# Optimization experiments

Measured on AMD Instinct MI355X. Metric: run time of the kernel, lower is better.

## Reference

```python
import jax, jax.numpy as jnp
import numpy as np

HEADS, DK, DV, STRIDE = 8, 32, 32, 2
EPS = 1e-5

def dwconv(x, w, b, stride):
    # depthwise 3x3, padding 1; w: [C,1,3,3]
    y = jax.lax.conv_general_dilated(
        x, w, (stride, stride), ((1, 1), (1, 1)),
        dimension_numbers=("NCHW", "OIHW", "NCHW"),
        feature_group_count=x.shape[1])
    return y + b[None, :, None, None]

def setup_inputs() -> dict:
    key = jax.random.key(0)
    ks = jax.random.split(key, 16)
    B_, C, H, W = 8, 256, 56, 56
    hd = HEADS * DK
    s = lambda k, shp: (jax.random.normal(k, shp, jnp.float32) * 0.02)
    return {
        "x": jax.random.normal(ks[0], (B_, C, H, W), jnp.float32),
        "Wk_dw": s(ks[1], (C, 1, 3, 3)), "bk_dw": jnp.zeros((C,), jnp.float32),
        "Wv_dw": s(ks[2], (C, 1, 3, 3)), "bv_dw": jnp.zeros((C,), jnp.float32),
        "Wq": s(ks[3], (hd, C)), "bq": jnp.zeros((hd,), jnp.float32),
        "Wk": s(ks[4], (hd, C)), "bk": jnp.zeros((hd,), jnp.float32),
        "Wv": s(ks[5], (HEADS * DV, C)), "bv": jnp.zeros((HEADS * DV,), jnp.float32),
        "Wo": s(ks[6], (C, HEADS * DV)), "bo": jnp.zeros((C,), jnp.float32),
        "Bbias": s(ks[7], (1, HEADS, H * W, (H // STRIDE) * (W // STRIDE))),
    }

def reference(x, Wk_dw, bk_dw, Wv_dw, bv_dw, Wq, bq, Wk, bk, Wv, bv, Wo, bo, Bbias):
    b, c, h, w = x.shape
    xr = x.reshape(b, c, h * w).transpose(0, 2, 1)  # [b, hw, c]
    # F.layer_norm with normalized_shape=(b, hw, c): single mean/var over ALL elements
    mu = jnp.mean(xr)
    var = jnp.mean((xr - mu) ** 2)
    xn = (xr - mu) * jax.lax.rsqrt(var + EPS)
    q = (xn @ Wq.T + bq).reshape(b, h * w, HEADS, DK).transpose(0, 2, 1, 3)  # [b,H,hw,dk]
    ki = dwconv(x, Wk_dw, bk_dw, STRIDE)
    kh, kw = ki.shape[2], ki.shape[3]
    kf = ki.reshape(b, c, kh * kw).transpose(0, 2, 1)
    k = (kf @ Wk.T + bk).reshape(b, kh * kw, HEADS, DK).transpose(0, 2, 1, 3)
    vi = dwconv(x, Wv_dw, bv_dw, STRIDE)
    vf = vi.reshape(b, c, kh * kw).transpose(0, 2, 1)
    v = (vf @ Wv.T + bv).reshape(b, kh * kw, HEADS, DV).transpose(0, 2, 1, 3)
    attn = jnp.einsum("bhid,bhjd->bhij", q, k) * (DK ** -0.5) + Bbias
    attn = jax.nn.softmax(attn, axis=-1)
    res = jnp.einsum("bhij,bhjd->bhid", attn, v).transpose(0, 2, 1, 3)
    res = res.reshape(b, h * w, HEADS * DV)
    out = (res @ Wo.T + bo).reshape(b, c, h, w)  # faithful to original .view (no transpose)
    return out + x
```

## Files before the change

### kernel.cpp

```cpp
#include <hip/hip_runtime.h>

typedef unsigned short u16;
typedef unsigned int   u32;
typedef __attribute__((ext_vector_type(8))) short short8;
typedef __attribute__((ext_vector_type(4))) float f32x4;

#define MFMA16(a, b, c) __builtin_amdgcn_mfma_f32_16x16x32_bf16((a), (b), (c), 0, 0, 0)

static constexpr int B_ = 8;
static constexpr int HW = 3136;
static constexpr int KW = 784;
static constexpr int NELEM = B_ * 256 * HW;

static constexpr size_t OFF_CNT = 4096;
static constexpr size_t OFF_W   = 8192;
static constexpr int AOFF_WQ = 0, AOFF_WK = 65536, AOFF_WV = 131072, AOFF_WO = 196608;
static constexpr int AOFF_WKDW = 262144, AOFF_WVDW = 264448;
static constexpr int AOFF_BKDW = 266752, AOFF_BVDW = 267008, AOFF_BQ = 267264;
static constexpr int AOFF_BK = 267520, AOFF_BV = 267776, AOFF_BO = 268032;
static constexpr size_t OFF_XT  = 557056;
static constexpr size_t SZ_XT   = (size_t)B_ * HW * 256 * 2;
static constexpr size_t SZ_KJ   = (size_t)B_ * KW * 256 * 2;
static constexpr size_t OFF_KIT = OFF_XT + SZ_XT;
static constexpr size_t OFF_VIT = OFF_KIT + SZ_KJ;
static constexpr size_t OFF_KI  = OFF_VIT + SZ_KJ;
static constexpr size_t OFF_VI  = OFF_KI + SZ_KJ;
static constexpr size_t OFF_Q   = OFF_VI + SZ_KJ;
static constexpr size_t OFF_O   = OFF_XT;

__device__ __forceinline__ float bf2f(u16 u) { return __uint_as_float(((u32)u) << 16); }
__device__ __forceinline__ u16 f2bf(float f) {
  u32 u = __float_as_uint(f);
  u32 r = u + 0x7FFFu + ((u >> 16) & 1u);
  return (u16)(r >> 16);
}
__device__ __forceinline__ float bflo(u32 u) { return __uint_as_float(u << 16); }
__device__ __forceinline__ float bfhi(u32 u) { return __uint_as_float(u & 0xFFFF0000u); }
__device__ __forceinline__ u32 packbf(float a, float b) {
  u32 ua = __float_as_uint(a); ua = (ua + 0x7FFFu + ((ua >> 16) & 1u)) >> 16;
  u32 ub = __float_as_uint(b); ub = (ub + 0x7FFFu + ((ub >> 16) & 1u)) >> 16;
  return ua | (ub << 16);
}

__global__ __launch_bounds__(256) void detect_k(const u32* __restrict__ x, int* __restrict__ cnt) {
  int c = 0;
  for (int i = threadIdx.x; i < 4096; i += 256) {
    float v = __uint_as_float(x[i] << 16);
    if (fabsf(v) > 1e4f) c++;
  }
#pragma unroll
  for (int off = 32; off > 0; off >>= 1) c += __shfl_down(c, off);
  if ((threadIdx.x & 63) == 0) atomicAdd(cnt, c);
}

struct CvtArgs { const void* src[12]; int dstoff[12]; int n[12]; };
__global__ __launch_bounds__(256) void cvtw_k(CvtArgs a, u16* __restrict__ arena,
                                              const int* __restrict__ cnt) {
  int t = blockIdx.y;
  int n = a.n[t];
  u16* d = arena + a.dstoff[t];
  int f32m = (*cnt >= 64);
  if (f32m) {
    const float* s = (const float*)a.src[t];
    for (int i = blockIdx.x * 256 + threadIdx.x; i < n; i += gridDim.x * 256) d[i] = f2bf(s[i]);
  } else {
    const u16* s = (const u16*)a.src[t];
    for (int i = blockIdx.x * 256 + threadIdx.x; i < n; i += gridDim.x * 256) d[i] = s[i];
  }
}

__global__ __launch_bounds__(256) void reduce_k(const void* __restrict__ x, double* __restrict__ acc,
                                                const int* __restrict__ cnt) {
  int f32m = (*cnt >= 64);
  float s = 0.f, ss = 0.f;
  if (f32m) {
    const float4* xv = (const float4*)x;
    const int n4 = NELEM / 4;
    for (int i = blockIdx.x * 256 + threadIdx.x; i < n4; i += gridDim.x * 256) {
      float4 u = xv[i];
      s += u.x + u.y + u.z + u.w;
      ss += u.x * u.x + u.y * u.y + u.z * u.z + u.w * u.w;
    }
  } else {
    const uint4* xv = (const uint4*)x;
    const int n8 = NELEM / 8;
    for (int i = blockIdx.x * 256 + threadIdx.x; i < n8; i += gridDim.x * 256) {
      uint4 u = xv[i];
      u32 w[4] = {u.x, u.y, u.z, u.w};
#pragma unroll
      for (int q = 0; q < 4; q++) {
        float f0 = __uint_as_float(w[q] << 16);
        float f1 = __uint_as_float(w[q] & 0xFFFF0000u);
        s += f0 + f1;
        ss += f0 * f0 + f1 * f1;
      }
    }
  }
#pragma unroll
  for (int off = 32; off > 0; off >>= 1) {
    s += __shfl_down(s, off);
    ss += __shfl_down(ss, off);
  }
  __shared__ float as_[4], ass_[4];
  int wv = threadIdx.x >> 6;
  if ((threadIdx.x & 63) == 0) { as_[wv] = s; ass_[wv] = ss; }
  __syncthreads();
  if (threadIdx.x == 0) {
    atomicAdd(acc + 0, (double)(as_[0] + as_[1] + as_[2] + as_[3]));
    atomicAdd(acc + 1, (double)(ass_[0] + ass_[1] + ass_[2] + ass_[3]));
  }
}

__global__ __launch_bounds__(256) void prep_k(const u16* __restrict__ wq, const u16* __restrict__ bq,
                                              float* __restrict__ wsf) {
  const double* acc = (const double*)wsf;
  __shared__ float sh[2];
  if (threadIdx.x == 0) {
    double N = (double)NELEM;
    double mu = acc[0] / N;
    double var = acc[1] / N - mu * mu;
    float rstd = (float)(1.0 / sqrt(var + 1e-5));
    sh[0] = (float)mu; sh[1] = rstd;
    wsf[4] = (float)mu; wsf[5] = rstd;
    wsf[6] = rstd * 0.17677669529663687f;
  }
  __syncthreads();
  int o = threadIdx.x;
  float wsum = 0.f;
  for (int c = 0; c < 256; c++) wsum += bf2f(wq[o * 256 + c]);
  wsf[16 + o] = (bf2f(bq[o]) - sh[1] * sh[0] * wsum) * 0.17677669529663687f;
}

__global__ __launch_bounds__(256) void transpose_x_k(const void* __restrict__ src, u16* __restrict__ dst,
                                                     const int* __restrict__ cnt) {
  int f32m = (*cnt >= 64);
  __shared__ u16 t[32][33];
  int b = blockIdx.z;
  int r0 = blockIdx.y * 32, c0 = blockIdx.x * 32;
  int tid = threadIdx.x, col = tid & 31;
  size_t base = (size_t)b * 256 * HW;
  if (f32m) {
    const float* s = (const float*)src + base;
#pragma unroll
    for (int i = 0; i < 4; i++) {
      int row = (tid >> 5) + i * 8;
      t[row][col] = f2bf(s[(size_t)(r0 + row) * HW + c0 + col]);
    }
  } else {
    const u16* s = (const u16*)src + base;
#pragma unroll
    for (int i = 0; i < 4; i++) {
      int row = (tid >> 5) + i * 8;
      t[row][col] = s[(size_t)(r0 + row) * HW + c0 + col];
    }
  }
  __syncthreads();
  u16* d = dst + base;
#pragma unroll
  for (int i = 0; i < 4; i++) {
    int row = (tid >> 5) + i * 8;
    d[(size_t)(c0 + row) * 256 + r0 + col] = t[col][row];
  }
}

__global__ __launch_bounds__(256) void transpose_kv_k(const u16* __restrict__ s1, u16* __restrict__ d1,
                                                      const u16* __restrict__ s2, u16* __restrict__ d2) {
  __shared__ u16 t[32][33];
  int which = blockIdx.z >> 3;
  int b = blockIdx.z & 7;
  const u16* src = which ? s2 : s1;
  u16* dst = which ? d2 : d1;
  int r0 = blockIdx.y * 32, c0 = blockIdx.x * 32;
  const u16* s = src + (size_t)b * 256 * KW;
  u16* d = dst + (size_t)b * 256 * KW;
  int tid = threadIdx.x, col = tid & 31;
#pragma unroll
  for (int i = 0; i < 4; i++) {
    int row = (tid >> 5) + i * 8;
    if (c0 + col < KW) t[row][col] = s[(size_t)(r0 + row) * KW + c0 + col];
  }
  __syncthreads();
#pragma unroll
  for (int i = 0; i < 4; i++) {
    int row = (tid >> 5) + i * 8;
    if (c0 + row < KW) d[(size_t)(c0 + row) * 256 + r0 + col] = t[col][row];
  }
}

__global__ __launch_bounds__(256) void dwconv_k(const void* __restrict__ x,
                                                const u16* __restrict__ arena,
                                                u16* __restrict__ ki, u16* __restrict__ vi,
                                                const int* __restrict__ cnt) {
  int f32m = (*cnt >= 64);
  int b = blockIdx.x >> 8;
  int c = blockIdx.x & 255;
  float wkf[9], wvf[9];
#pragma unroll
  for (int t = 0; t < 9; t++) {
    wkf[t] = bf2f(arena[AOFF_WKDW + c * 9 + t]);
    wvf[t] = bf2f(arena[AOFF_WVDW + c * 9 + t]);
  }
  float kb = bf2f(arena[AOFF_BKDW + c]), vb = bf2f(arena[AOFF_BVDW + c]);
  size_t xbase = (size_t)(b * 256 + c) * HW;
  auto body = [&](auto LDX) {
    for (int j = threadIdx.x; j < KW; j += 256) {
      int oi = j / 28, oj = j % 28;
      float ka = kb, va = vb;
#pragma unroll
      for (int di = 0; di < 3; di++) {
        int ii = 2 * oi - 1 + di;
        if ((unsigned)ii >= 56u) continue;
#pragma unroll
        for (int dj = 0; dj < 3; dj++) {
          int ij = 2 * oj - 1 + dj;
          if ((unsigned)ij >= 56u) continue;
          float xv = LDX(ii * 56 + ij);
          ka += xv * wkf[di * 3 + dj];
          va += xv * wvf[di * 3 + dj];
        }
      }
      ki[(size_t)(b * 256 + c) * KW + j] = f2bf(ka);
      vi[(size_t)(b * 256 + c) * KW + j] = f2bf(va);
    }
  };
  if (f32m) {
    const float* xp = (const float*)x + xbase;
    body([&](int i) { return xp[i]; });
  } else {
    const u16* xp = (const u16*)x + xbase;
    body([&](int i) { return bf2f(xp[i]); });
  }
}

template<int MODE>
__global__ __launch_bounds__(256, 4) void proj2_k(const u16* __restrict__ act, const u16* __restrict__ Wt,
                                                  const float* __restrict__ wsf, const u16* __restrict__ bias,
                                                  const void* __restrict__ x, void* __restrict__ outp,
                                                  const int* __restrict__ cnt, int R, int tpb) {
  __shared__ __align__(16) u16 Wl[64 * 264];
  int tid = threadIdx.x, lane = tid & 63, wave = tid >> 6;
  int l15 = lane & 15, quad = lane >> 4;
  int og = blockIdx.x & 3;
  int tmp = blockIdx.x >> 2;
  int qc = tmp % 7, b = tmp / 7;
  {
    int row = tid >> 2, cb = (tid & 3) * 64;
    const u16* wsrc = Wt + (size_t)(og * 64 + row) * 256 + cb;
#pragma unroll
    for (int i = 0; i < 8; i++)
      *(short8*)&Wl[row * 264 + cb + i * 8] = *(const short8*)(wsrc + i * 8);
  }
  __syncthreads();
  int f32m = (MODE == 2) ? (*cnt >= 64) : 0;
  float alpha = (MODE == 0) ? wsf[6] : 0.f;
  for (int tt = wave; tt < tpb; tt += 4) {
    int p0 = (qc * tpb + tt) * 16;
    const u16* arow = act + ((size_t)b * R + p0 + l15) * 256 + quad * 8;
    short8 afr[8];
#pragma unroll
    for (int ks = 0; ks < 8; ks++) afr[ks] = *(const short8*)(arow + ks * 32);
#pragma unroll
    for (int ot = 0; ot < 4; ot++) {
      f32x4 acc = {0.f, 0.f, 0.f, 0.f};
#pragma unroll
      for (int ks = 0; ks < 8; ks++) {
        short8 bfr = *(const short8*)&Wl[(ot * 16 + l15) * 264 + ks * 32 + quad * 8];
        acc = MFMA16(afr[ks], bfr, acc);
      }
      int o = og * 64 + ot * 16 + l15;
      if (MODE == 0) {
        float bet = wsf[16 + o];
        u16* q = (u16*)outp;
#pragma unroll
        for (int r = 0; r < 4; r++)
          q[((size_t)b * R + p0 + quad * 4 + r) * 256 + o] = f2bf(alpha * acc[r] + bet);
      } else if (MODE == 1) {
        float bi = bf2f(bias[o]);
        u16* ko = (u16*)outp;
#pragma unroll
        for (int r = 0; r < 4; r++)
          ko[((size_t)b * R + p0 + quad * 4 + r) * 256 + o] = f2bf(acc[r] + bi);
      } else {
        float bi = bf2f(bias[o]);
        if (f32m) {
          const float* xf = (const float*)x;
          float* of = (float*)outp;
#pragma unroll
          for (int r = 0; r < 4; r++) {
            size_t idx = ((size_t)b * R + p0 + quad * 4 + r) * 256 + o;
            of[idx] = acc[r] + bi + xf[idx];
          }
        } else {
          const u16* xb = (const u16*)x;
          u16* ob_ = (u16*)outp;
#pragma unroll
          for (int r = 0; r < 4; r++) {
            size_t idx = ((size_t)b * R + p0 + quad * 4 + r) * 256 + o;
            ob_[idx] = f2bf(acc[r] + bi + bf2f(xb[idx]));
          }
        }
      }
    }
  }
}

__global__ __launch_bounds__(256) void proj_v_k(const u16* __restrict__ Wv, const u16* __restrict__ vit,
                                                const u16* __restrict__ bv, u16* __restrict__ vT) {
  int lane = threadIdx.x & 63, wave = threadIdx.x >> 6;
  int l15 = lane & 15, quad = lane >> 4;
  int b = blockIdx.x >> 4;
  int ob = (blockIdx.x >> 2) & 3;
  int js = blockIdx.x & 3;
  int o0 = ob * 64 + wave * 16;
  const u16* arow = Wv + (size_t)(o0 + l15) * 256 + quad * 8;
  short8 af[8];
#pragma unroll
  for (int ks = 0; ks < 8; ks++) af[ks] = *(const short8*)(arow + ks * 32);
  int jt0 = js * 13;
  int jt1 = (jt0 + 13 < 49) ? jt0 + 13 : 49;
  for (int jt = jt0; jt < jt1; jt++) {
    const u16* brow = vit + ((size_t)(b * KW) + jt * 16 + l15) * 256 + quad * 8;
    f32x4 acc = {0.f, 0.f, 0.f, 0.f};
#pragma unroll
    for (int ks = 0; ks < 8; ks++) acc = MFMA16(af[ks], *(const short8*)(brow + ks * 32), acc);
#pragma unroll
    for (int r = 0; r < 4; r++) {
      int o = o0 + quad * 4 + r;
      vT[((size_t)(b * 256) + o) * KW + jt * 16 + l15] = f2bf(acc[r] + bf2f(bv[o]));
    }
  }
}

static constexpr int PSTRIDE = 136;
__global__ __launch_bounds__(256, 3) void attn_k(const u16* __restrict__ q, const u16* __restrict__ k,
                                                 const u16* __restrict__ vT, const void* __restrict__ Bb,
                                                 u16* __restrict__ Ob, const int* __restrict__ cnt) {
  int f32m = (*cnt >= 64);
  int tid = threadIdx.x;
  int lane = tid & 63, wave = tid >> 6;
  int l15 = lane & 15, quad = lane >> 4;
  int bid = blockIdx.x;
  int pt = bid >> 4;
  int h = (bid >> 1) & 7;
  int half = bid & 1;
  int b = half * 4 + wave;
  int p0 = pt * 16;
  __shared__ __align__(16) u16 blsT[784 * 16];
  __shared__ __align__(16) u16 Pch[4][16 * PSTRIDE];

  {
    size_t boff = ((size_t)(h * HW) + p0) * KW;
    if (f32m) {
      const float* bbf = (const float*)Bb + boff;
#pragma unroll
      for (int it = 0; it < 13; it++) {
        int chunk = it * 256 + tid;
        if (chunk < 3136) {
          int row = chunk / 196, c4 = (chunk - row * 196) * 4;
          float4 v = *(const float4*)(bbf + (size_t)row * KW + c4);
          blsT[(c4 + 0) * 16 + row] = f2bf(v.x);
          blsT[(c4 + 1) * 16 + row] = f2bf(v.y);
          blsT[(c4 + 2) * 16 + row] = f2bf(v.z);
          blsT[(c4 + 3) * 16 + row] = f2bf(v.w);
        }
      }
    } else {
      const u16* bbb = (const u16*)Bb + boff;
#pragma unroll
      for (int it = 0; it < 13; it++) {
        int chunk = it * 256 + tid;
        if (chunk < 3136) {
          int row = chunk / 196, c4 = (chunk - row * 196) * 4;
          uint2 lv = *(const uint2*)(bbb + (size_t)row * KW + c4);
          blsT[(c4 + 0) * 16 + row] = (u16)(lv.x & 0xFFFFu);
          blsT[(c4 + 1) * 16 + row] = (u16)(lv.x >> 16);
          blsT[(c4 + 2) * 16 + row] = (u16)(lv.y & 0xFFFFu);
          blsT[(c4 + 3) * 16 + row] = (u16)(lv.y >> 16);
        }
      }
    }
  }
  __syncthreads();

  const u16* qp = q + ((size_t)(b * HW) + p0 + l15) * 256 + h * 32 + quad * 8;
  short8 af = *(const short8*)qp;
  const u16* kb = k + (size_t)b * KW * 256 + h * 32 + quad * 8;
  const u16* vb = vT + ((size_t)(b * 256) + h * 32) * KW;
  u16* pw = &Pch[wave][0];

  float m[4], l[4];
  f32x4 oa = {0.f, 0.f, 0.f, 0.f}, oc = {0.f, 0.f, 0.f, 0.f};
#pragma unroll
  for (int r = 0; r < 4; r++) { m[r] = -3.0e38f; l[r] = 0.f; }

#pragma unroll 1
  for (int c = 0; c < 7; c++) {
    f32x4 s[8];
#pragma unroll
    for (int t = 0; t < 8; t++) {
      int jt = c * 8 + t;
      int jrow = jt * 16 + l15;
      int jcl = jrow > 783 ? 783 : jrow;
      short8 kf = *(const short8*)(kb + (size_t)jcl * 256);
      f32x4 acc = {0.f, 0.f, 0.f, 0.f};
      acc = MFMA16(af, kf, acc);
      uint2 braw = *(const uint2*)&blsT[jcl * 16 + quad * 4];
      bool valid = jrow < 784;
      s[t][0] = valid ? acc[0] + bflo(braw.x) : -3.0e38f;
      s[t][1] = valid ? acc[1] + bfhi(braw.x) : -3.0e38f;
      s[t][2] = valid ? acc[2] + bflo(braw.y) : -3.0e38f;
      s[t][3] = valid ? acc[3] + bfhi(braw.y) : -3.0e38f;
    }
    float cm[4], al[4], ps[4];
#pragma unroll
    for (int r = 0; r < 4; r++) {
      float v = s[0][r];
#pragma unroll
      for (int t = 1; t < 8; t++) v = fmaxf(v, s[t][r]);
      cm[r] = v;
    }
#pragma unroll
    for (int off = 1; off < 16; off <<= 1)
#pragma unroll
      for (int r = 0; r < 4; r++) cm[r] = fmaxf(cm[r], __shfl_xor(cm[r], off));
#pragma unroll
    for (int r = 0; r < 4; r++) {
      float mn = fmaxf(m[r], cm[r]);
      al[r] = __expf(m[r] - mn);
      m[r] = mn;
      ps[r] = 0.f;
    }
#pragma unroll
    for (int t = 0; t < 8; t++)
#pragma unroll
      for (int r = 0; r < 4; r++) {
        float e = __expf(s[t][r] - m[r]);
        s[t][r] = e;
        ps[r] += e;
      }
#pragma unroll
    for (int off = 1; off < 16; off <<= 1)
#pragma unroll
      for (int r = 0; r < 4; r++) ps[r] += __shfl_xor(ps[r], off);
#pragma unroll
    for (int r = 0; r < 4; r++) {
      l[r] = l[r] * al[r] + ps[r];
      oa[r] *= al[r];
      oc[r] *= al[r];
    }
#pragma unroll
    for (int t = 0; t < 8; t++) {
      int col = t * 16 + l15;
#pragma unroll
      for (int r = 0; r < 4; r++)
        pw[(quad * 4 + r) * PSTRIDE + col] = f2bf(s[t][r]);
    }
    __builtin_amdgcn_s_waitcnt(0xC07F);
#pragma unroll
    for (int kc = 0; kc < 4; kc++) {
      short8 pf = *(const short8*)(pw + l15 * PSTRIDE + kc * 32 + quad * 8);
      int jo = c * 128 + kc * 32 + quad * 8;
      if (jo > 776) jo = 776;
      short8 v0 = *(const short8*)(vb + (size_t)l15 * KW + jo);
      short8 v1 = *(const short8*)(vb + (size_t)(16 + l15) * KW + jo);
      oa = MFMA16(pf, v0, oa);
      oc = MFMA16(pf, v1, oc);
    }
  }

  size_t obase = ((size_t)(b * HW) + p0 + quad * 4) * 256 + h * 32 + l15;
#pragma unroll
  for (int r = 0; r < 4; r++) {
    float inv = 1.f / l[r];
    Ob[obase + (size_t)r * 256]      = f2bf(oa[r] * inv);
    Ob[obase + (size_t)r * 256 + 16] = f2bf(oc[r] * inv);
  }
}

extern "C" void kernel_launch(void* const* d_in, const int* in_sizes, int n_in,
                              void* d_out, int out_size, void* d_ws, size_t ws_size,
                              hipStream_t stream) {
  (void)in_sizes; (void)n_in; (void)out_size; (void)ws_size;
  const void* x = d_in[0];
  char* ws = (char*)d_ws;
  int* cnt = (int*)(ws + OFF_CNT);
  u16* arena = (u16*)(ws + OFF_W);
  u16* xt  = (u16*)(ws + OFF_XT);
  u16* kit = (u16*)(ws + OFF_KIT);
  u16* vit = (u16*)(ws + OFF_VIT);
  u16* ki  = (u16*)(ws + OFF_KI);
  u16* vi  = (u16*)(ws + OFF_VI);
  u16* qb  = (u16*)(ws + OFF_Q);
  u16* Obuf = (u16*)(ws + OFF_O);

  CvtArgs a;
  const int srcidx[12] = {5, 7, 9, 11, 1, 3, 2, 4, 6, 8, 10, 12};
  const int dofs[12] = {AOFF_WQ, AOFF_WK, AOFF_WV, AOFF_WO, AOFF_WKDW, AOFF_WVDW,
                        AOFF_BKDW, AOFF_BVDW, AOFF_BQ, AOFF_BK, AOFF_BV, AOFF_BO};
  const int ns[12] = {65536, 65536, 65536, 65536, 2304, 2304, 256, 256, 256, 256, 256, 256};
  for (int i = 0; i < 12; i++) { a.src[i] = d_in[srcidx[i]]; a.dstoff[i] = dofs[i]; a.n[i] = ns[i]; }

  hipMemsetAsync(d_ws, 0, 8192, stream);
  detect_k<<<1, 256, 0, stream>>>((const u32*)x, cnt);
  cvtw_k<<<dim3(32, 12), 256, 0, stream>>>(a, arena, cnt);
  reduce_k<<<1024, 256, 0, stream>>>(x, (double*)d_ws, cnt);
  prep_k<<<1, 256, 0, stream>>>(arena + AOFF_WQ, arena + AOFF_BQ, (float*)d_ws);
  transpose_x_k<<<dim3(98, 8, 8), 256, 0, stream>>>(x, xt, cnt);
  dwconv_k<<<2048, 256, 0, stream>>>(x, arena, ki, vi, cnt);
  transpose_kv_k<<<dim3(25, 8, 16), 256, 0, stream>>>(ki, kit, vi, vit);
  proj2_k<1><<<224, 256, 0, stream>>>(kit, arena + AOFF_WK, nullptr, arena + AOFF_BK,
                                      nullptr, ki, cnt, KW, 7);
  proj_v_k<<<128, 256, 0, stream>>>(arena + AOFF_WV, vit, arena + AOFF_BV, vi);
  proj2_k<0><<<224, 256, 0, stream>>>(xt, arena + AOFF_WQ, (const float*)d_ws, nullptr,
                                      nullptr, qb, cnt, HW, 28);
  attn_k<<<3136, 256, 0, stream>>>(qb, ki, vi, d_in[13], Obuf, cnt);
  proj2_k<2><<<224, 256, 0, stream>>>(Obuf, arena + AOFF_WO, nullptr, arena + AOFF_BO,
                                      x, d_out, cnt, HW, 28);
}
```

Before: 531.7 us.

## Fuse stats into transpose, inline dtype detect, drop bias LDS staging in attention

Removes the memset, detect and reduce kernels: the dtype check becomes a per-wave ballot inside each kernel, and the layer-norm sum and sum of squares are computed as block partials in the x transpose and reduced in prep. The attention kernel no longer stages the bias tile transposed in shared memory and instead loads bias directly from global per score. It also raises the attention occupancy hint to 6, writes the softmax probabilities to LDS in the same loop as the exponentials, and doubles the grid for the Q and output projections. Direct strided global bias loads may cost more bandwidth than the staged copy did, in exchange for lower LDS use and higher occupancy.

Result: slower. 780.1 us (+46.7%).

```diff
diff --git a/kernel.cpp b/kernel.cpp
--- a/kernel.cpp
+++ b/kernel.cpp
@@ -2,6 +2,7 @@
 
 typedef unsigned short u16;
 typedef unsigned int   u32;
+typedef unsigned long long u64;
 typedef __attribute__((ext_vector_type(8))) short short8;
 typedef __attribute__((ext_vector_type(4))) float f32x4;
 
@@ -10,15 +11,14 @@
 static constexpr int B_ = 8;
 static constexpr int HW = 3136;
 static constexpr int KW = 784;
-static constexpr int NELEM = B_ * 256 * HW;
-
-static constexpr size_t OFF_CNT = 4096;
-static constexpr size_t OFF_W   = 8192;
+
+static constexpr size_t OFF_PART = 4096;
+static constexpr size_t OFF_W   = 131072;
 static constexpr int AOFF_WQ = 0, AOFF_WK = 65536, AOFF_WV = 131072, AOFF_WO = 196608;
 static constexpr int AOFF_WKDW = 262144, AOFF_WVDW = 264448;
 static constexpr int AOFF_BKDW = 266752, AOFF_BVDW = 267008, AOFF_BQ = 267264;
 static constexpr int AOFF_BK = 267520, AOFF_BV = 267776, AOFF_BO = 268032;
-static constexpr size_t OFF_XT  = 557056;
+static constexpr size_t OFF_XT  = 688128;
 static constexpr size_t SZ_XT   = (size_t)B_ * HW * 256 * 2;
 static constexpr size_t SZ_KJ   = (size_t)B_ * KW * 256 * 2;
 static constexpr size_t OFF_KIT = OFF_XT + SZ_XT;
@@ -36,30 +36,21 @@
 }
 __device__ __forceinline__ float bflo(u32 u) { return __uint_as_float(u << 16); }
 __device__ __forceinline__ float bfhi(u32 u) { return __uint_as_float(u & 0xFFFF0000u); }
-__device__ __forceinline__ u32 packbf(float a, float b) {
-  u32 ua = __float_as_uint(a); ua = (ua + 0x7FFFu + ((ua >> 16) & 1u)) >> 16;
-  u32 ub = __float_as_uint(b); ub = (ub + 0x7FFFu + ((ub >> 16) & 1u)) >> 16;
-  return ua | (ub << 16);
-}
-
-__global__ __launch_bounds__(256) void detect_k(const u32* __restrict__ x, int* __restrict__ cnt) {
-  int c = 0;
-  for (int i = threadIdx.x; i < 4096; i += 256) {
-    float v = __uint_as_float(x[i] << 16);
-    if (fabsf(v) > 1e4f) c++;
-  }
-#pragma unroll
-  for (int off = 32; off > 0; off >>= 1) c += __shfl_down(c, off);
-  if ((threadIdx.x & 63) == 0) atomicAdd(cnt, c);
+
+__device__ __forceinline__ int detect_f32(const u32* __restrict__ ref) {
+  int lane = threadIdx.x & 63;
+  float v = __uint_as_float(ref[lane] << 16);
+  u64 b = __ballot(fabsf(v) > 1e4f);
+  return __popcll(b) >= 4;
 }
 
 struct CvtArgs { const void* src[12]; int dstoff[12]; int n[12]; };
 __global__ __launch_bounds__(256) void cvtw_k(CvtArgs a, u16* __restrict__ arena,
-                                              const int* __restrict__ cnt) {
+                                              const u32* __restrict__ xw) {
+  int f32m = detect_f32(xw);
   int t = blockIdx.y;
   int n = a.n[t];
   u16* d = arena + a.dstoff[t];
-  int f32m = (*cnt >= 64);
   if (f32m) {
     const float* s = (const float*)a.src[t];
     for (int i = blockIdx.x * 256 + threadIdx.x; i < n; i += gridDim.x * 256) d[i] = f2bf(s[i]);
@@ -69,89 +60,33 @@
   }
 }
 
-__global__ __launch_bounds__(256) void reduce_k(const void* __restrict__ x, double* __restrict__ acc,
-                                                const int* __restrict__ cnt) {
-  int f32m = (*cnt >= 64);
-  float s = 0.f, ss = 0.f;
-  if (f32m) {
-    const float4* xv = (const float4*)x;
-    const int n4 = NELEM / 4;
-    for (int i = blockIdx.x * 256 + threadIdx.x; i < n4; i += gridDim.x * 256) {
-      float4 u = xv[i];
-      s += u.x + u.y + u.z + u.w;
-      ss += u.x * u.x + u.y * u.y + u.z * u.z + u.w * u.w;
-    }
-  } else {
-    const uint4* xv = (const uint4*)x;
-    const int n8 = NELEM / 8;
-    for (int i = blockIdx.x * 256 + threadIdx.x; i < n8; i += gridDim.x * 256) {
-      uint4 u = xv[i];
-      u32 w[4] = {u.x, u.y, u.z, u.w};
-#pragma unroll
-      for (int q = 0; q < 4; q++) {
-        float f0 = __uint_as_float(w[q] << 16);
-        float f1 = __uint_as_float(w[q] & 0xFFFF0000u);
-        s += f0 + f1;
-        ss += f0 * f0 + f1 * f1;
-      }
-    }
-  }
-#pragma unroll
-  for (int off = 32; off > 0; off >>= 1) {
-    s += __shfl_down(s, off);
-    ss += __shfl_down(ss, off);
-  }
-  __shared__ float as_[4], ass_[4];
-  int wv = threadIdx.x >> 6;
-  if ((threadIdx.x & 63) == 0) { as_[wv] = s; ass_[wv] = ss; }
-  __syncthreads();
-  if (threadIdx.x == 0) {
-    atomicAdd(acc + 0, (double)(as_[0] + as_[1] + as_[2] + as_[3]));
-    atomicAdd(acc + 1, (double)(ass_[0] + ass_[1] + ass_[2] + ass_[3]));
-  }
-}
-
-__global__ __launch_bounds__(256) void prep_k(const u16* __restrict__ wq, const u16* __restrict__ bq,
-                                              float* __restrict__ wsf) {
-  const double* acc = (const double*)wsf;
-  __shared__ float sh[2];
-  if (threadIdx.x == 0) {
-    double N = (double)NELEM;
-    double mu = acc[0] / N;
-    double var = acc[1] / N - mu * mu;
-    float rstd = (float)(1.0 / sqrt(var + 1e-5));
-    sh[0] = (float)mu; sh[1] = rstd;
-    wsf[4] = (float)mu; wsf[5] = rstd;
-    wsf[6] = rstd * 0.17677669529663687f;
-  }
-  __syncthreads();
-  int o = threadIdx.x;
-  float wsum = 0.f;
-  for (int c = 0; c < 256; c++) wsum += bf2f(wq[o * 256 + c]);
-  wsf[16 + o] = (bf2f(bq[o]) - sh[1] * sh[0] * wsum) * 0.17677669529663687f;
-}
-
 __global__ __launch_bounds__(256) void transpose_x_k(const void* __restrict__ src, u16* __restrict__ dst,
-                                                     const int* __restrict__ cnt) {
-  int f32m = (*cnt >= 64);
+                                                     float2* __restrict__ part) {
+  int f32m = detect_f32((const u32*)src);
   __shared__ u16 t[32][33];
   int b = blockIdx.z;
   int r0 = blockIdx.y * 32, c0 = blockIdx.x * 32;
   int tid = threadIdx.x, col = tid & 31;
   size_t base = (size_t)b * 256 * HW;
+  float s = 0.f, ss = 0.f;
   if (f32m) {
-    const float* s = (const float*)src + base;
+    const float* sp = (const float*)src + base;
 #pragma unroll
     for (int i = 0; i < 4; i++) {
       int row = (tid >> 5) + i * 8;
-      t[row][col] = f2bf(s[(size_t)(r0 + row) * HW + c0 + col]);
+      float v = sp[(size_t)(r0 + row) * HW + c0 + col];
+      t[row][col] = f2bf(v);
+      s += v; ss += v * v;
     }
   } else {
-    const u16* s = (const u16*)src + base;
+    const u16* sp = (const u16*)src + base;
 #pragma unroll
     for (int i = 0; i < 4; i++) {
       int row = (tid >> 5) + i * 8;
-      t[row][col] = s[(size_t)(r0 + row) * HW + c0 + col];
+      u16 raw = sp[(size_t)(r0 + row) * HW + c0 + col];
+      t[row][col] = raw;
+      float v = bf2f(raw);
+      s += v; ss += v * v;
     }
   }
   __syncthreads();
@@ -161,6 +96,52 @@
     int row = (tid >> 5) + i * 8;
     d[(size_t)(c0 + row) * 256 + r0 + col] = t[col][row];
   }
+#pragma unroll
+  for (int off = 32; off > 0; off >>= 1) {
+    s += __shfl_down(s, off);
+    ss += __shfl_down(ss, off);
+  }
+  __shared__ float rs[4], rss[4];
+  if ((tid & 63) == 0) { rs[tid >> 6] = s; rss[tid >> 6] = ss; }
+  __syncthreads();
+  if (tid == 0) {
+    int idx = (blockIdx.z * gridDim.y + blockIdx.y) * gridDim.x + blockIdx.x;
+    part[idx] = make_float2(rs[0] + rs[1] + rs[2] + rs[3], rss[0] + rss[1] + rss[2] + rss[3]);
+  }
+}
+
+__global__ __launch_bounds__(256) void prep_k(const u16* __restrict__ wq, const u16* __restrict__ bq,
+                                              const float2* __restrict__ part, float* __restrict__ wsf) {
+  double s = 0.0, ss = 0.0;
+  for (int i = threadIdx.x; i < 6272; i += 256) {
+    float2 p = part[i];
+    s += (double)p.x; ss += (double)p.y;
+  }
+#pragma unroll
+  for (int off = 32; off > 0; off >>= 1) {
+    s += __shfl_down(s, off);
+    ss += __shfl_down(ss, off);
+  }
+  __shared__ double ds[4], dss[4];
+  __shared__ float sh[2];
+  int tid = threadIdx.x;
+  if ((tid & 63) == 0) { ds[tid >> 6] = s; dss[tid >> 6] = ss; }
+  __syncthreads();
+  if (tid == 0) {
+    double S = ds[0] + ds[1] + ds[2] + ds[3];
+    double SS = dss[0] + dss[1] + dss[2] + dss[3];
+    double N = (double)B_ * 256 * HW;
+    double mu = S / N;
+    double var = SS / N - mu * mu;
+    float rstd = (float)(1.0 / sqrt(var + 1e-5));
+    sh[0] = (float)mu; sh[1] = rstd;
+    wsf[6] = rstd * 0.17677669529663687f;
+  }
+  __syncthreads();
+  int o = tid;
+  float wsum = 0.f;
+  for (int c = 0; c < 256; c++) wsum += bf2f(wq[o * 256 + c]);
+  wsf[16 + o] = (bf2f(bq[o]) - sh[1] * sh[0] * wsum) * 0.17677669529663687f;
 }
 
 __global__ __launch_bounds__(256) void transpose_kv_k(const u16* __restrict__ s1, u16* __restrict__ d1,
@@ -189,9 +170,8 @@
 
 __global__ __launch_bounds__(256) void dwconv_k(const void* __restrict__ x,
                                                 const u16* __restrict__ arena,
-                                                u16* __restrict__ ki, u16* __restrict__ vi,
-                                                const int* __restrict__ cnt) {
-  int f32m = (*cnt >= 64);
+                                                u16* __restrict__ ki, u16* __restrict__ vi) {
+  int f32m = detect_f32((const u32*)x);
   int b = blockIdx.x >> 8;
   int c = blockIdx.x & 255;
   float wkf[9], wvf[9];
@@ -236,13 +216,13 @@
 __global__ __launch_bounds__(256, 4) void proj2_k(const u16* __restrict__ act, const u16* __restrict__ Wt,
                                                   const float* __restrict__ wsf, const u16* __restrict__ bias,
                                                   const void* __restrict__ x, void* __restrict__ outp,
-                                                  const int* __restrict__ cnt, int R, int tpb) {
+                                                  int R, int tpb, int qcN) {
   __shared__ __align__(16) u16 Wl[64 * 264];
   int tid = threadIdx.x, lane = tid & 63, wave = tid >> 6;
   int l15 = lane & 15, quad = lane >> 4;
   int og = blockIdx.x & 3;
   int tmp = blockIdx.x >> 2;
-  int qc = tmp % 7, b = tmp / 7;
+  int qc = tmp % qcN, b = tmp / qcN;
   {
     int row = tid >> 2, cb = (tid & 3) * 64;
     const u16* wsrc = Wt + (size_t)(og * 64 + row) * 256 + cb;
@@ -251,7 +231,7 @@
       *(short8*)&Wl[row * 264 + cb + i * 8] = *(const short8*)(wsrc + i * 8);
   }
   __syncthreads();
-  int f32m = (MODE == 2) ? (*cnt >= 64) : 0;
+  int f32m = (MODE == 2) ? detect_f32((const u32*)x) : 0;
   float alpha = (MODE == 0) ? wsf[6] : 0.f;
   for (int tt = wave; tt < tpb; tt += 4) {
     int p0 = (qc * tpb + tt) * 16;
@@ -332,10 +312,10 @@
 }
 
 static constexpr int PSTRIDE = 136;
-__global__ __launch_bounds__(256, 3) void attn_k(const u16* __restrict__ q, const u16* __restrict__ k,
+__global__ __launch_bounds__(256, 6) void attn_k(const u16* __restrict__ q, const u16* __restrict__ k,
                                                  const u16* __restrict__ vT, const void* __restrict__ Bb,
-                                                 u16* __restrict__ Ob, const int* __restrict__ cnt) {
-  int f32m = (*cnt >= 64);
+                                                 u16* __restrict__ Ob) {
+  int f32m = detect_f32((const u32*)Bb);
   int tid = threadIdx.x;
   int lane = tid & 63, wave = tid >> 6;
   int l15 = lane & 15, quad = lane >> 4;
@@ -345,48 +325,16 @@
   int half = bid & 1;
   int b = half * 4 + wave;
   int p0 = pt * 16;
-  __shared__ __align__(16) u16 blsT[784 * 16];
   __shared__ __align__(16) u16 Pch[4][16 * PSTRIDE];
-
-  {
-    size_t boff = ((size_t)(h * HW) + p0) * KW;
-    if (f32m) {
-      const float* bbf = (const float*)Bb + boff;
-#pragma unroll
-      for (int it = 0; it < 13; it++) {
-        int chunk = it * 256 + tid;
-        if (chunk < 3136) {
-          int row = chunk / 196, c4 = (chunk - row * 196) * 4;
-          float4 v = *(const float4*)(bbf + (size_t)row * KW + c4);
-          blsT[(c4 + 0) * 16 + row] = f2bf(v.x);
-          blsT[(c4 + 1) * 16 + row] = f2bf(v.y);
-          blsT[(c4 + 2) * 16 + row] = f2bf(v.z);
-          blsT[(c4 + 3) * 16 + row] = f2bf(v.w);
-        }
-      }
-    } else {
-      const u16* bbb = (const u16*)Bb + boff;
-#pragma unroll
-      for (int it = 0; it < 13; it++) {
-        int chunk = it * 256 + tid;
-        if (chunk < 3136) {
-          int row = chunk / 196, c4 = (chunk - row * 196) * 4;
-          uint2 lv = *(const uint2*)(bbb + (size_t)row * KW + c4);
-          blsT[(c4 + 0) * 16 + row] = (u16)(lv.x & 0xFFFFu);
-          blsT[(c4 + 1) * 16 + row] = (u16)(lv.x >> 16);
-          blsT[(c4 + 2) * 16 + row] = (u16)(lv.y & 0xFFFFu);
-          blsT[(c4 + 3) * 16 + row] = (u16)(lv.y >> 16);
-        }
-      }
-    }
-  }
-  __syncthreads();
 
   const u16* qp = q + ((size_t)(b * HW) + p0 + l15) * 256 + h * 32 + quad * 8;
   short8 af = *(const short8*)qp;
   const u16* kb = k + (size_t)b * KW * 256 + h * 32 + quad * 8;
   const u16* vb = vT + ((size_t)(b * 256) + h * 32) * KW;
   u16* pw = &Pch[wave][0];
+  size_t boff = ((size_t)(h * HW) + p0 + quad * 4) * KW;
+  const float* bbf = (const float*)Bb + boff;
+  const u16* bbb = (const u16*)Bb + boff;
 
   float m[4], l[4];
   f32x4 oa = {0.f, 0.f, 0.f, 0.f}, oc = {0.f, 0.f, 0.f, 0.f};
@@ -404,12 +352,18 @@
       short8 kf = *(const short8*)(kb + (size_t)jcl * 256);
       f32x4 acc = {0.f, 0.f, 0.f, 0.f};
       acc = MFMA16(af, kf, acc);
-      uint2 braw = *(const uint2*)&blsT[jcl * 16 + quad * 4];
+      float b0, b1, b2, b3;
+      if (f32m) {
+        b0 = bbf[jcl]; b1 = bbf[KW + jcl]; b2 = bbf[2 * KW + jcl]; b3 = bbf[3 * KW + jcl];
+      } else {
+        b0 = bf2f(bbb[jcl]); b1 = bf2f(bbb[KW + jcl]);
+        b2 = bf2f(bbb[2 * KW + jcl]); b3 = bf2f(bbb[3 * KW + jcl]);
+      }
       bool valid = jrow < 784;
-      s[t][0] = valid ? acc[0] + bflo(braw.x) : -3.0e38f;
-      s[t][1] = valid ? acc[1] + bfhi(braw.x) : -3.0e38f;
-      s[t][2] = valid ? acc[2] + bflo(braw.y) : -3.0e38f;
-      s[t][3] = valid ? acc[3] + bfhi(braw.y) : -3.0e38f;
+      s[t][0] = valid ? acc[0] + b0 : -3.0e38f;
+      s[t][1] = valid ? acc[1] + b1 : -3.0e38f;
+      s[t][2] = valid ? acc[2] + b2 : -3.0e38f;
+      s[t][3] = valid ? acc[3] + b3 : -3.0e38f;
     }
     float cm[4], al[4], ps[4];
 #pragma unroll
@@ -431,13 +385,15 @@
       ps[r] = 0.f;
     }
 #pragma unroll
-    for (int t = 0; t < 8; t++)
+    for (int t = 0; t < 8; t++) {
+      int col = t * 16 + l15;
 #pragma unroll
       for (int r = 0; r < 4; r++) {
         float e = __expf(s[t][r] - m[r]);
-        s[t][r] = e;
+        pw[(quad * 4 + r) * PSTRIDE + col] = f2bf(e);
         ps[r] += e;
       }
+    }
 #pragma unroll
     for (int off = 1; off < 16; off <<= 1)
 #pragma unroll
@@ -447,13 +403,6 @@
       l[r] = l[r] * al[r] + ps[r];
       oa[r] *= al[r];
       oc[r] *= al[r];
-    }
-#pragma unroll
-    for (int t = 0; t < 8; t++) {
-      int col = t * 16 + l15;
-#pragma unroll
-      for (int r = 0; r < 4; r++)
-        pw[(quad * 4 + r) * PSTRIDE + col] = f2bf(s[t][r]);
     }
     __builtin_amdgcn_s_waitcnt(0xC07F);
 #pragma unroll
@@ -483,7 +432,8 @@
   (void)in_sizes; (void)n_in; (void)out_size; (void)ws_size;
   const void* x = d_in[0];
   char* ws = (char*)d_ws;
-  int* cnt = (int*)(ws + OFF_CNT);
+  float2* part = (float2*)(ws + OFF_PART);
+  float* wsf = (float*)ws;
   u16* arena = (u16*)(ws + OFF_W);
   u16* xt  = (u16*)(ws + OFF_XT);
   u16* kit = (u16*)(ws + OFF_KIT);
@@ -500,20 +450,17 @@
   const int ns[12] = {65536, 65536, 65536, 65536, 2304, 2304, 256, 256, 256, 256, 256, 256};
   for (int i = 0; i < 12; i++) { a.src[i] = d_in[srcidx[i]]; a.dstoff[i] = dofs[i]; a.n[i] = ns[i]; }
 
-  hipMemsetAsync(d_ws, 0, 8192, stream);
-  detect_k<<<1, 256, 0, stream>>>((const u32*)x, cnt);
-  cvtw_k<<<dim3(32, 12), 256, 0, stream>>>(a, arena, cnt);
-  reduce_k<<<1024, 256, 0, stream>>>(x, (double*)d_ws, cnt);
-  prep_k<<<1, 256, 0, stream>>>(arena + AOFF_WQ, arena + AOFF_BQ, (float*)d_ws);
-  transpose_x_k<<<dim3(98, 8, 8), 256, 0, stream>>>(x, xt, cnt);
-  dwconv_k<<<2048, 256, 0, stream>>>(x, arena, ki, vi, cnt);
+  cvtw_k<<<dim3(32, 12), 256, 0, stream>>>(a, arena, (const u32*)x);
+  transpose_x_k<<<dim3(98, 8, 8), 256, 0, stream>>>(x, xt, part);
+  prep_k<<<1, 256, 0, stream>>>(arena + AOFF_WQ, arena + AOFF_BQ, part, wsf);
+  dwconv_k<<<2048, 256, 0, stream>>>(x, arena, ki, vi);
   transpose_kv_k<<<dim3(25, 8, 16), 256, 0, stream>>>(ki, kit, vi, vit);
-  proj2_k<1><<<224, 256, 0, stream>>>(kit, arena + AOFF_WK, nullptr, arena + AOFF_BK,
-                                      nullptr, ki, cnt, KW, 7);
+  proj2_k<1><<<224, 256, 0, stream>>>(kit, arena + AOFF_WK, wsf, arena + AOFF_BK,
+                                      nullptr, ki, KW, 7, 7);
   proj_v_k<<<128, 256, 0, stream>>>(arena + AOFF_WV, vit, arena + AOFF_BV, vi);
-  proj2_k<0><<<224, 256, 0, stream>>>(xt, arena + AOFF_WQ, (const float*)d_ws, nullptr,
-                                      nullptr, qb, cnt, HW, 28);
-  attn_k<<<3136, 256, 0, stream>>>(qb, ki, vi, d_in[13], Obuf, cnt);
-  proj2_k<2><<<224, 256, 0, stream>>>(Obuf, arena + AOFF_WO, nullptr, arena + AOFF_BO,
-                                      x, d_out, cnt, HW, 28);
-}
+  proj2_k<0><<<448, 256, 0, stream>>>(xt, arena + AOFF_WQ, wsf, nullptr,
+                                      nullptr, qb, HW, 14, 14);
+  attn_k<<<3136, 256, 0, stream>>>(qb, ki, vi, d_in[13], Obuf);
+  proj2_k<2><<<448, 256, 0, stream>>>(Obuf, arena + AOFF_WO, wsf, arena + AOFF_BO,
+                                      x, d_out, HW, 14, 14);
+}
```
